# Kernel optimization log

Measured on AMD Instinct MI355X. Metric: run time of the kernel, lower is better.

Reference implementation:

```python
import jax, jax.numpy as jnp
import numpy as np

N_NODES = 50000
HEADS = 3
C = 64  # node_channels
NEG_SLOPE = 0.2


def setup_inputs() -> dict:
    key = jax.random.key(0)
    ks = jax.random.split(key, 8)
    E = 800000
    x = jax.random.normal(ks[0], (N_NODES, C), dtype=jnp.float32)
    edge_index = jax.random.randint(ks[1], (2, E), 0, N_NODES, dtype=jnp.int64)
    edge_attr = jax.random.normal(ks[2], (E, 16), dtype=jnp.float32)
    weight_node = jax.random.normal(ks[3], (C, HEADS * C), dtype=jnp.float32) * 0.1
    weight_edge = jax.random.normal(ks[4], (16, HEADS * C), dtype=jnp.float32) * 0.1
    weight_triplet_att = jax.random.normal(ks[5], (1, HEADS, 3 * C), dtype=jnp.float32) * 0.1
    weight_scale = jax.random.normal(ks[6], (HEADS * C, C), dtype=jnp.float32) * 0.1
    bias = jnp.zeros((C,), dtype=jnp.float32)
    return {"x": x, "edge_index": edge_index, "edge_attr": edge_attr,
            "weight_node": weight_node, "weight_edge": weight_edge,
            "weight_triplet_att": weight_triplet_att,
            "weight_scale": weight_scale, "bias": bias}


def reference(x, edge_index, edge_attr, weight_node, weight_edge,
              weight_triplet_att, weight_scale, bias):
    E = edge_index.shape[1]
    src = edge_index[0]  # j (source)
    dst = edge_index[1]  # i (target, softmax/aggregation index)

    x_proj = x @ weight_node              # [N, H*C]
    e = edge_attr @ weight_edge           # [E, H*C]

    x_j = x_proj[src].reshape(E, HEADS, C)
    x_i = x_proj[dst].reshape(E, HEADS, C)
    e_ij = e.reshape(E, HEADS, C)

    # attention weights split over the triplet concat [x_i | e_ij | x_j]
    w = weight_triplet_att.reshape(HEADS, 3, C)  # [H,3,C]
    alpha = (jnp.einsum('ehc,hc->eh', x_i, w[:, 0])
             + jnp.einsum('ehc,hc->eh', e_ij, w[:, 1])
             + jnp.einsum('ehc,hc->eh', x_j, w[:, 2]))  # [E,H]
    alpha = jnp.where(alpha >= 0, alpha, NEG_SLOPE * alpha)  # leaky_relu

    # scatter-softmax over incoming edges of each target node
    m = jax.ops.segment_max(alpha, dst, num_segments=N_NODES)  # [N,H]
    m = jnp.where(jnp.isfinite(m), m, 0.0)
    exp_a = jnp.exp(alpha - m[dst])
    denom = jax.ops.segment_sum(exp_a, dst, num_segments=N_NODES)  # [N,H]
    alpha = exp_a / (denom[dst] + 1e-16)

    msg = alpha[:, :, None] * e_ij * x_j  # [E,H,C]
    aggr = jax.ops.segment_sum(msg.reshape(E, HEADS * C), dst,
                               num_segments=N_NODES)  # [N,H*C]
    return aggr @ weight_scale + bias
```

## Files before the change

kernel.cpp:

```cpp
#include <hip/hip_runtime.h>
#include <hip/hip_bf16.h>


#define N_NODES 50000
#define CCH 64
#define HEADS 3
#define HC 192
#define NEG_SLOPE 0.2f
#define NWAVES 12288

typedef _Float16 h2 __attribute__((ext_vector_type(2)));
__device__ __forceinline__ h2 uh(unsigned u) {
    union { unsigned u; h2 h; } x; x.u = u; return x.h;
}
__device__ __forceinline__ unsigned hu(float a, float b) {
    union { unsigned u; _Float16 h[2]; } x;
    x.h[0] = (_Float16)a; x.h[1] = (_Float16)b; return x.u;
}

__global__ __launch_bounds__(256) void k_hist(const int* __restrict__ ei,
                                              int* __restrict__ cnt,
                                              const float* __restrict__ We,
                                              const float* __restrict__ Watt,
                                              float* __restrict__ v1, int E) {
    int e = blockIdx.x * 256 + threadIdx.x;
    if (e < E) atomicAdd(&cnt[ei[E + e]], 1);
    if (blockIdx.x == 0 && threadIdx.x < HEADS * 16) {
        int h = threadIdx.x / 16, k = threadIdx.x % 16;
        float s = 0.f;
        #pragma unroll
        for (int c = 0; c < CCH; ++c)
            s = fmaf(We[k * HC + h * CCH + c], Watt[h * HC + CCH + c], s);
        v1[threadIdx.x] = s;
    }
}

__global__ __launch_bounds__(192) void k_xproj(
    const float* __restrict__ x, const float* __restrict__ Wn,
    const float* __restrict__ Watt, uint2* __restrict__ xph2,
    float* __restrict__ a0, float* __restrict__ a2) {
    __shared__ _Float16 pack[16 * CCH * 4];
    int t = threadIdx.x;
    float wreg[CCH];
    #pragma unroll
    for (int k = 0; k < CCH; ++k) wreg[k] = Wn[k * HC + t];
    int base = blockIdx.x * 16;
    int h = t >> 6, c = t & 63;
    float w0 = Watt[h * HC + c];
    float w2 = Watt[h * HC + 2 * CCH + c];
    int jmax = N_NODES - base; jmax = jmax > 16 ? 16 : jmax;
    #pragma unroll 1
    for (int j = 0; j < jmax; ++j) {
        const float* xr = x + (size_t)(base + j) * CCH;
        float val = 0.f;
        #pragma unroll
        for (int k = 0; k < CCH; ++k) val = fmaf(xr[k], wreg[k], val);
        pack[(j * CCH + c) * 4 + h] = (_Float16)val;
        if (h == 0) pack[(j * CCH + c) * 4 + 3] = (_Float16)0.f;
        float p0 = val * w0, p2 = val * w2;
        #pragma unroll
        for (int off = 32; off; off >>= 1) {
            p0 += __shfl_down(p0, off);
            p2 += __shfl_down(p2, off);
        }
        if (c == 0) {
            a0[(base + j) * HEADS + h] = p0;
            a2[(base + j) * HEADS + h] = p2;
        }
    }
    __syncthreads();
    const uint2* p2v = (const uint2*)pack;
    for (int i = t; i < 16 * CCH; i += 192) {
        int n = base + (i >> 6);
        if (n < N_NODES) xph2[(size_t)base * CCH + i] = p2v[i];
    }
}

__global__ __launch_bounds__(1024) void k_bsum(const int* __restrict__ cnt,
                                               int* __restrict__ bsum) {
    __shared__ int ws[16];
    int t = threadIdx.x, lane = t & 63, wid = t >> 6;
    int i = blockIdx.x * 1024 + t;
    int v = (i < N_NODES) ? cnt[i] : 0;
    #pragma unroll
    for (int o = 32; o; o >>= 1) v += __shfl_down(v, o);
    if (lane == 0) ws[wid] = v;
    __syncthreads();
    if (wid == 0) {
        int s = (lane < 16) ? ws[lane] : 0;
        #pragma unroll
        for (int o = 8; o; o >>= 1) s += __shfl_down(s, o);
        if (lane == 0) bsum[blockIdx.x] = s;
    }
}

__global__ __launch_bounds__(1024) void k_fin(const int* __restrict__ cnt,
                                              const int* __restrict__ bsum,
                                              int* __restrict__ off,
                                              int* __restrict__ cursor) {
    __shared__ int ws[16];
    __shared__ int bof_s;
    int t = threadIdx.x, lane = t & 63, wid = t >> 6;
    int i = blockIdx.x * 1024 + t;
    int v = (i < N_NODES) ? cnt[i] : 0;
    int x = v;
    #pragma unroll
    for (int o = 1; o < 64; o <<= 1) {
        int y = __shfl_up(x, o);
        if (lane >= o) x += y;
    }
    if (lane == 63) ws[wid] = x;
    __syncthreads();
    if (wid == 0) {
        int s = (lane < 16) ? ws[lane] : 0;
        #pragma unroll
        for (int o = 1; o < 16; o <<= 1) {
            int y = __shfl_up(s, o);
            if (lane >= o) s += y;
        }
        if (lane < 16) ws[lane] = s;
    } else if (wid == 1) {
        int bv = (lane < 49) ? bsum[lane] : 0;
        int bx = bv;
        #pragma unroll
        for (int o = 1; o < 64; o <<= 1) {
            int y = __shfl_up(bx, o);
            if (lane >= o) bx += y;
        }
        if (lane == (int)blockIdx.x) bof_s = bx - bv;
        if (blockIdx.x == 48 && lane == 48) off[N_NODES] = bx;
    }
    __syncthreads();
    int excl = bof_s + (wid ? ws[wid - 1] : 0) + x - v;
    if (i < N_NODES) { off[i] = excl; cursor[i] = excl; }
}

__global__ __launch_bounds__(256) void k_part(const int* __restrict__ off,
                                              int* __restrict__ wstart, int E) {
    int w = blockIdx.x * 256 + threadIdx.x;
    if (w > NWAVES) return;
    if (w == NWAVES) { wstart[NWAVES] = N_NODES; return; }
    long tgt = (long)E * w / NWAVES;
    int lo = 0, hi = N_NODES;
    while (lo < hi) {
        int mid = (lo + hi) >> 1;
        if (off[mid] < (int)tgt) lo = mid + 1; else hi = mid;
    }
    wstart[w] = lo;
}

__global__ __launch_bounds__(256) void k_place(
    const int* __restrict__ ei, const float* __restrict__ ea,
    const float* __restrict__ a0, const float* __restrict__ a2,
    const float* __restrict__ v1, int* __restrict__ cursor,
    float* __restrict__ recs, int E) {
    int e = blockIdx.x * 256 + threadIdx.x;
    if (e >= E) return;
    int src = ei[e], dst = ei[E + e];
    const float4* q = (const float4*)(ea + (size_t)e * 16);
    float4 q0 = q[0], q1 = q[1], q2 = q[2], q3 = q[3];
    float at[16] = {q0.x, q0.y, q0.z, q0.w, q1.x, q1.y, q1.z, q1.w,
                    q2.x, q2.y, q2.z, q2.w, q3.x, q3.y, q3.z, q3.w};
    float ex[HEADS];
    #pragma unroll
    for (int h = 0; h < HEADS; ++h) {
        float s = a0[dst * HEADS + h] + a2[src * HEADS + h];
        #pragma unroll
        for (int j = 0; j < 16; ++j) s = fmaf(at[j], v1[h * 16 + j], s);
        s = (s >= 0.f) ? s : NEG_SLOPE * s;
        ex[h] = __expf(s);
    }
    int pos = atomicAdd(&cursor[dst], 1);
    float* rp = recs + (size_t)pos * 12;
    uint4 r0 = {hu(at[0], at[1]), hu(at[2], at[3]), hu(at[4], at[5]), hu(at[6], at[7])};
    uint4 r1 = {hu(at[8], at[9]), hu(at[10], at[11]), hu(at[12], at[13]), hu(at[14], at[15])};
    float4 r2 = {ex[0], ex[1], ex[2], __int_as_float(src)};
    *(uint4*)rp = r0;
    *(uint4*)(rp + 4) = r1;
    *(float4*)(rp + 8) = r2;
}

__global__ __launch_bounds__(256, 6) void k_msg(
    const int* __restrict__ off, const int* __restrict__ wstart,
    const float* __restrict__ recs, const uint2* __restrict__ xph2,
    const float* __restrict__ We, _Float16* __restrict__ rowsH) {
    int lane = threadIdx.x & 63;
    int w = blockIdx.x * 4 + (threadIdx.x >> 6);
    #define WP(h, q) hu(We[(2*(q)) * HC + (h) * CCH + lane], \
                        We[(2*(q)+1) * HC + (h) * CCH + lane])
    unsigned w00 = WP(0,0), w01 = WP(0,1), w02 = WP(0,2), w03 = WP(0,3),
             w04 = WP(0,4), w05 = WP(0,5), w06 = WP(0,6), w07 = WP(0,7);
    unsigned w10 = WP(1,0), w11 = WP(1,1), w12 = WP(1,2), w13 = WP(1,3),
             w14 = WP(1,4), w15 = WP(1,5), w16 = WP(1,6), w17 = WP(1,7);
    unsigned w20 = WP(2,0), w21 = WP(2,1), w22 = WP(2,2), w23 = WP(2,3),
             w24 = WP(2,4), w25 = WP(2,5), w26 = WP(2,6), w27 = WP(2,7);
    #undef WP

    int n0 = wstart[w], n1 = wstart[w + 1];
    n0 = __builtin_amdgcn_readfirstlane(n0);
    n1 = __builtin_amdgcn_readfirstlane(n1);
    if (n0 >= n1) return;

    int n = n0;
    int k    = __builtin_amdgcn_readfirstlane(off[n0]);
    int kend = __builtin_amdgcn_readfirstlane(off[n1]);
    int re   = __builtin_amdgcn_readfirstlane(off[n0 + 1]);

    float acc0 = 0.f, acc1 = 0.f, acc2 = 0.f;
    float den0 = 0.f, den1 = 0.f, den2 = 0.f;

    uint4 U0, U1; float4 RX; uint2 xv;
    if (k < kend) {
        const float* rp = recs + (size_t)k * 12;
        U0 = *(const uint4*)rp;
        U1 = *(const uint4*)(rp + 4);
        RX = *(const float4*)(rp + 8);
        int src = __builtin_amdgcn_readfirstlane(__float_as_int(RX.w));
        xv = xph2[(size_t)src * CCH + lane];
    }

    #define FLUSH(nn)                                                      \
        {                                                                  \
            size_t ro = (size_t)(nn) * HC + lane;                          \
            rowsH[ro]           = (_Float16)(acc0 / (den0 + 1e-16f));      \
            rowsH[ro + CCH]     = (_Float16)(acc1 / (den1 + 1e-16f));      \
            rowsH[ro + 2 * CCH] = (_Float16)(acc2 / (den2 + 1e-16f));      \
            acc0 = acc1 = acc2 = den0 = den1 = den2 = 0.f;                 \
        }

    while (k < kend) {
        while (k == re) {
            FLUSH(n);
            ++n;
            re = __builtin_amdgcn_readfirstlane(off[n + 1]);
        }
        int kn = (k + 1 < kend) ? k + 1 : k;
        const float* rpn = recs + (size_t)kn * 12;
        uint4 U0n = *(const uint4*)rpn;
        uint4 U1n = *(const uint4*)(rpn + 4);
        float4 RXn = *(const float4*)(rpn + 8);
        float ev0 = 0.f, ev1 = 0.f, ev2 = 0.f;
        #define D(u, wv, acc) acc = __builtin_amdgcn_fdot2(uh(u), uh(wv), acc, false);
        D(U0.x, w00, ev0) D(U0.x, w10, ev1) D(U0.x, w20, ev2)
        D(U0.y, w01, ev0) D(U0.y, w11, ev1) D(U0.y, w21, ev2)
        D(U0.z, w02, ev0) D(U0.z, w12, ev1) D(U0.z, w22, ev2)
        D(U0.w, w03, ev0) D(U0.w, w13, ev1) D(U0.w, w23, ev2)
        D(U1.x, w04, ev0) D(U1.x, w14, ev1) D(U1.x, w24, ev2)
        D(U1.y, w05, ev0) D(U1.y, w15, ev1) D(U1.y, w25, ev2)
        D(U1.z, w06, ev0) D(U1.z, w16, ev1) D(U1.z, w26, ev2)
        D(U1.w, w07, ev0) D(U1.w, w17, ev1) D(U1.w, w27, ev2)
        #undef D
        h2 xa = uh(xv.x), xb = uh(xv.y);
        den0 += RX.x; den1 += RX.y; den2 += RX.z;
        acc0 = fmaf(RX.x * ev0, (float)xa.x, acc0);
        acc1 = fmaf(RX.y * ev1, (float)xa.y, acc1);
        acc2 = fmaf(RX.z * ev2, (float)xb.x, acc2);
        U0 = U0n; U1 = U1n; RX = RXn;
        int src_n = __builtin_amdgcn_readfirstlane(__float_as_int(RXn.w));
        xv = xph2[(size_t)src_n * CCH + lane];
        ++k;
    }
    FLUSH(n);
    while (++n < n1) FLUSH(n);
    #undef FLUSH
}

__global__ __launch_bounds__(256) void k_out(
    const _Float16* __restrict__ rowsH, const float* __restrict__ Ws,
    const float* __restrict__ bias, float* __restrict__ out) {
    int lane = threadIdx.x & 63;
    int wgid = __builtin_amdgcn_readfirstlane(blockIdx.x * 4 + (threadIdx.x >> 6));
    float b = bias[lane];
    #define WQ(q) hu(Ws[(2*(q)) * CCH + lane], Ws[(2*(q)+1) * CCH + lane])
    unsigned s00=WQ(0),  s01=WQ(1),  s02=WQ(2),  s03=WQ(3),  s04=WQ(4),  s05=WQ(5),  s06=WQ(6),  s07=WQ(7);
    unsigned s08=WQ(8),  s09=WQ(9),  s10=WQ(10), s11=WQ(11), s12=WQ(12), s13=WQ(13), s14=WQ(14), s15=WQ(15);
    unsigned s16=WQ(16), s17=WQ(17), s18=WQ(18), s19=WQ(19), s20=WQ(20), s21=WQ(21), s22=WQ(22), s23=WQ(23);
    unsigned s24=WQ(24), s25=WQ(25), s26=WQ(26), s27=WQ(27), s28=WQ(28), s29=WQ(29), s30=WQ(30), s31=WQ(31);
    unsigned s32=WQ(32), s33=WQ(33), s34=WQ(34), s35=WQ(35), s36=WQ(36), s37=WQ(37), s38=WQ(38), s39=WQ(39);
    unsigned s40=WQ(40), s41=WQ(41), s42=WQ(42), s43=WQ(43), s44=WQ(44), s45=WQ(45), s46=WQ(46), s47=WQ(47);
    unsigned s48=WQ(48), s49=WQ(49), s50=WQ(50), s51=WQ(51), s52=WQ(52), s53=WQ(53), s54=WQ(54), s55=WQ(55);
    unsigned s56=WQ(56), s57=WQ(57), s58=WQ(58), s59=WQ(59), s60=WQ(60), s61=WQ(61), s62=WQ(62), s63=WQ(63);
    unsigned s64=WQ(64), s65=WQ(65), s66=WQ(66), s67=WQ(67), s68=WQ(68), s69=WQ(69), s70=WQ(70), s71=WQ(71);
    unsigned s72=WQ(72), s73=WQ(73), s74=WQ(74), s75=WQ(75), s76=WQ(76), s77=WQ(77), s78=WQ(78), s79=WQ(79);
    unsigned s80=WQ(80), s81=WQ(81), s82=WQ(82), s83=WQ(83), s84=WQ(84), s85=WQ(85), s86=WQ(86), s87=WQ(87);
    unsigned s88=WQ(88), s89=WQ(89), s90=WQ(90), s91=WQ(91), s92=WQ(92), s93=WQ(93), s94=WQ(94), s95=WQ(95);
    #undef WQ
    #pragma unroll 1
    for (int n = wgid; n < N_NODES; n += 1024) {
        const unsigned* rp = (const unsigned*)(rowsH + (size_t)n * HC);
        float a0_ = b, a1_ = 0.f, a2_ = 0.f, a3_ = 0.f;
        #define DQ(q, sreg, acc) acc = __builtin_amdgcn_fdot2(uh(rp[q]), uh(sreg), acc, false);
        DQ(0,s00,a0_)  DQ(1,s01,a1_)  DQ(2,s02,a2_)  DQ(3,s03,a3_)
        DQ(4,s04,a0_)  DQ(5,s05,a1_)  DQ(6,s06,a2_)  DQ(7,s07,a3_)
        DQ(8,s08,a0_)  DQ(9,s09,a1_)  DQ(10,s10,a2_) DQ(11,s11,a3_)
        DQ(12,s12,a0_) DQ(13,s13,a1_) DQ(14,s14,a2_) DQ(15,s15,a3_)
        DQ(16,s16,a0_) DQ(17,s17,a1_) DQ(18,s18,a2_) DQ(19,s19,a3_)
        DQ(20,s20,a0_) DQ(21,s21,a1_) DQ(22,s22,a2_) DQ(23,s23,a3_)
        DQ(24,s24,a0_) DQ(25,s25,a1_) DQ(26,s26,a2_) DQ(27,s27,a3_)
        DQ(28,s28,a0_) DQ(29,s29,a1_) DQ(30,s30,a2_) DQ(31,s31,a3_)
        DQ(32,s32,a0_) DQ(33,s33,a1_) DQ(34,s34,a2_) DQ(35,s35,a3_)
        DQ(36,s36,a0_) DQ(37,s37,a1_) DQ(38,s38,a2_) DQ(39,s39,a3_)
        DQ(40,s40,a0_) DQ(41,s41,a1_) DQ(42,s42,a2_) DQ(43,s43,a3_)
        DQ(44,s44,a0_) DQ(45,s45,a1_) DQ(46,s46,a2_) DQ(47,s47,a3_)
        DQ(48,s48,a0_) DQ(49,s49,a1_) DQ(50,s50,a2_) DQ(51,s51,a3_)
        DQ(52,s52,a0_) DQ(53,s53,a1_) DQ(54,s54,a2_) DQ(55,s55,a3_)
        DQ(56,s56,a0_) DQ(57,s57,a1_) DQ(58,s58,a2_) DQ(59,s59,a3_)
        DQ(60,s60,a0_) DQ(61,s61,a1_) DQ(62,s62,a2_) DQ(63,s63,a3_)
        DQ(64,s64,a0_) DQ(65,s65,a1_) DQ(66,s66,a2_) DQ(67,s67,a3_)
        DQ(68,s68,a0_) DQ(69,s69,a1_) DQ(70,s70,a2_) DQ(71,s71,a3_)
        DQ(72,s72,a0_) DQ(73,s73,a1_) DQ(74,s74,a2_) DQ(75,s75,a3_)
        DQ(76,s76,a0_) DQ(77,s77,a1_) DQ(78,s78,a2_) DQ(79,s79,a3_)
        DQ(80,s80,a0_) DQ(81,s81,a1_) DQ(82,s82,a2_) DQ(83,s83,a3_)
        DQ(84,s84,a0_) DQ(85,s85,a1_) DQ(86,s86,a2_) DQ(87,s87,a3_)
        DQ(88,s88,a0_) DQ(89,s89,a1_) DQ(90,s90,a2_) DQ(91,s91,a3_)
        DQ(92,s92,a0_) DQ(93,s93,a1_) DQ(94,s94,a2_) DQ(95,s95,a3_)
        #undef DQ
        out[(size_t)n * CCH + lane] = (a0_ + a1_) + (a2_ + a3_);
    }
}

extern "C" void kernel_launch(void* const* d_in, const int* in_sizes, int n_in,
                              void* d_out, int out_size, void* d_ws, size_t ws_size,
                              hipStream_t stream) {
    const float* x    = (const float*)d_in[0];
    const int*   ei   = (const int*)d_in[1];
    const float* ea   = (const float*)d_in[2];
    const float* Wn   = (const float*)d_in[3];
    const float* We   = (const float*)d_in[4];
    const float* Watt = (const float*)d_in[5];
    const float* Ws   = (const float*)d_in[6];
    const float* bias = (const float*)d_in[7];
    float* out = (float*)d_out;

    const int E = in_sizes[1] / 2;

    char* w = (char*)d_ws;
    size_t o = 0;
    int*   cnt    = (int*)(w + o);    o += 50048 * 4;
    int*   off    = (int*)(w + o);    o += 50064 * 4;
    int*   cursor = (int*)(w + o);    o += 50048 * 4;
    int*   wst    = (int*)(w + o);    o += (NWAVES + 16) * 4;
    int*   bsum   = (int*)(w + o);    o += 64 * 4;
    float* v1     = (float*)(w + o);  o += 64 * 4;
    float* a0     = (float*)(w + o);  o += 150016 * 4;
    float* a2     = (float*)(w + o);  o += 150016 * 4;
    uint2* xph2   = (uint2*)(w + o);  o += (size_t)N_NODES * CCH * 8;
    _Float16* rowsH = (_Float16*)(w + o); o += (size_t)N_NODES * HC * 2;
    float* recs   = (float*)(w + o);  o += (size_t)E * 48;

    hipMemsetAsync(cnt, 0, 50048 * 4, stream);

    k_hist<<<(E + 255) / 256, 256, 0, stream>>>(ei, cnt, We, Watt, v1, E);
    k_xproj<<<(N_NODES + 15) / 16, 192, 0, stream>>>(x, Wn, Watt, xph2, a0, a2);
    k_bsum<<<49, 1024, 0, stream>>>(cnt, bsum);
    k_fin<<<49, 1024, 0, stream>>>(cnt, bsum, off, cursor);
    k_part<<<(NWAVES + 256) / 256, 256, 0, stream>>>(off, wst, E);
    k_place<<<(E + 255) / 256, 256, 0, stream>>>(ei, ea, a0, a2, v1, cursor, recs, E);
    k_msg<<<NWAVES / 4, 256, 0, stream>>>(off, wst, recs, xph2, We, rowsH);
    k_out<<<256, 256, 0, stream>>>(rowsH, Ws, bias, out);
}
```

Measured before the change: 377.2 us.

## Merge histogram with node projection and fuse scan stages via grid barrier

Folds the degree histogram and v1 precompute into the node projection kernel as extra blocks, and fuses the block-sum, prefix-scan finish and wave partition kernels into one 49-block kernel that uses a software grid barrier. This cuts the launch count from eight to five and removes the gaps between small dependent kernels. The grid barrier assumes all 49 blocks are co-resident, which holds on this GPU, and it adds atomic spin waiting.

```diff
diff --git a/kernel.cpp b/kernel.cpp
--- a/kernel.cpp
+++ b/kernel.cpp
@@ -8,6 +8,8 @@
 #define HC 192
 #define NEG_SLOPE 0.2f
 #define NWAVES 12288
+#define NBX 3125
+#define NSCAN 49
 
 typedef _Float16 h2 __attribute__((ext_vector_type(2)));
 __device__ __forceinline__ h2 uh(unsigned u) {
@@ -18,33 +20,45 @@
     x.h[0] = (_Float16)a; x.h[1] = (_Float16)b; return x.u;
 }
 
-__global__ __launch_bounds__(256) void k_hist(const int* __restrict__ ei,
-                                              int* __restrict__ cnt,
-                                              const float* __restrict__ We,
-                                              const float* __restrict__ Watt,
-                                              float* __restrict__ v1, int E) {
-    int e = blockIdx.x * 256 + threadIdx.x;
-    if (e < E) atomicAdd(&cnt[ei[E + e]], 1);
-    if (blockIdx.x == 0 && threadIdx.x < HEADS * 16) {
-        int h = threadIdx.x / 16, k = threadIdx.x % 16;
-        float s = 0.f;
-        #pragma unroll
-        for (int c = 0; c < CCH; ++c)
-            s = fmaf(We[k * HC + h * CCH + c], Watt[h * HC + CCH + c], s);
-        v1[threadIdx.x] = s;
-    }
-}
-
-__global__ __launch_bounds__(192) void k_xproj(
+__device__ __forceinline__ void gbar(int* bar, int phase, int nb) {
+    __syncthreads();
+    if (threadIdx.x == 0) {
+        __threadfence();
+        __hip_atomic_fetch_add(&bar[phase], 1, __ATOMIC_ACQ_REL,
+                               __HIP_MEMORY_SCOPE_AGENT);
+        while (__hip_atomic_load(&bar[phase], __ATOMIC_ACQUIRE,
+                                 __HIP_MEMORY_SCOPE_AGENT) < nb) {}
+        __threadfence();
+    }
+    __syncthreads();
+}
+
+__global__ __launch_bounds__(192) void k_front(
     const float* __restrict__ x, const float* __restrict__ Wn,
     const float* __restrict__ Watt, uint2* __restrict__ xph2,
-    float* __restrict__ a0, float* __restrict__ a2) {
+    float* __restrict__ a0, float* __restrict__ a2,
+    const int* __restrict__ ei, int* __restrict__ cnt,
+    const float* __restrict__ We, float* __restrict__ v1, int E) {
+    int t = threadIdx.x;
+    int bx = blockIdx.x;
+    if (bx >= NBX) {
+        int e = (bx - NBX) * 192 + t;
+        if (e < E) atomicAdd(&cnt[ei[E + e]], 1);
+        if (bx == NBX && t < HEADS * 16) {
+            int h = t / 16, k = t % 16;
+            float s = 0.f;
+            #pragma unroll
+            for (int c = 0; c < CCH; ++c)
+                s = fmaf(We[k * HC + h * CCH + c], Watt[h * HC + CCH + c], s);
+            v1[t] = s;
+        }
+        return;
+    }
     __shared__ _Float16 pack[16 * CCH * 4];
-    int t = threadIdx.x;
     float wreg[CCH];
     #pragma unroll
     for (int k = 0; k < CCH; ++k) wreg[k] = Wn[k * HC + t];
-    int base = blockIdx.x * 16;
+    int base = bx * 16;
     int h = t >> 6, c = t & 63;
     float w0 = Watt[h * HC + c];
     float w2 = Watt[h * HC + 2 * CCH + c];
@@ -76,33 +90,29 @@
     }
 }
 
-__global__ __launch_bounds__(1024) void k_bsum(const int* __restrict__ cnt,
-                                               int* __restrict__ bsum) {
-    __shared__ int ws[16];
-    int t = threadIdx.x, lane = t & 63, wid = t >> 6;
-    int i = blockIdx.x * 1024 + t;
-    int v = (i < N_NODES) ? cnt[i] : 0;
-    #pragma unroll
-    for (int o = 32; o; o >>= 1) v += __shfl_down(v, o);
-    if (lane == 0) ws[wid] = v;
-    __syncthreads();
-    if (wid == 0) {
-        int s = (lane < 16) ? ws[lane] : 0;
-        #pragma unroll
-        for (int o = 8; o; o >>= 1) s += __shfl_down(s, o);
-        if (lane == 0) bsum[blockIdx.x] = s;
-    }
-}
-
-__global__ __launch_bounds__(1024) void k_fin(const int* __restrict__ cnt,
-                                              const int* __restrict__ bsum,
-                                              int* __restrict__ off,
-                                              int* __restrict__ cursor) {
+__global__ __launch_bounds__(1024) void k_scan49(
+    const int* __restrict__ cnt, int* __restrict__ off, int* __restrict__ cursor,
+    int* __restrict__ wstart, int* __restrict__ bar, int* __restrict__ bsum,
+    int E) {
     __shared__ int ws[16];
     __shared__ int bof_s;
-    int t = threadIdx.x, lane = t & 63, wid = t >> 6;
-    int i = blockIdx.x * 1024 + t;
+    int b = blockIdx.x, t = threadIdx.x, lane = t & 63, wid = t >> 6;
+    int i = b * 1024 + t;
     int v = (i < N_NODES) ? cnt[i] : 0;
+    {
+        int r = v;
+        #pragma unroll
+        for (int o = 32; o; o >>= 1) r += __shfl_down(r, o);
+        if (lane == 0) ws[wid] = r;
+        __syncthreads();
+        if (wid == 0) {
+            int s = (lane < 16) ? ws[lane] : 0;
+            #pragma unroll
+            for (int o = 8; o; o >>= 1) s += __shfl_down(s, o);
+            if (lane == 0) bsum[b] = s;
+        }
+    }
+    gbar(bar, 0, NSCAN);
     int x = v;
     #pragma unroll
     for (int o = 1; o < 64; o <<= 1) {
@@ -120,33 +130,33 @@
         }
         if (lane < 16) ws[lane] = s;
     } else if (wid == 1) {
-        int bv = (lane < 49) ? bsum[lane] : 0;
+        int bv = (lane < NSCAN) ? bsum[lane] : 0;
         int bx = bv;
         #pragma unroll
         for (int o = 1; o < 64; o <<= 1) {
             int y = __shfl_up(bx, o);
             if (lane >= o) bx += y;
         }
-        if (lane == (int)blockIdx.x) bof_s = bx - bv;
-        if (blockIdx.x == 48 && lane == 48) off[N_NODES] = bx;
+        if (lane == b) bof_s = bx - bv;
     }
     __syncthreads();
     int excl = bof_s + (wid ? ws[wid - 1] : 0) + x - v;
     if (i < N_NODES) { off[i] = excl; cursor[i] = excl; }
-}
-
-__global__ __launch_bounds__(256) void k_part(const int* __restrict__ off,
-                                              int* __restrict__ wstart, int E) {
-    int w = blockIdx.x * 256 + threadIdx.x;
-    if (w > NWAVES) return;
-    if (w == NWAVES) { wstart[NWAVES] = N_NODES; return; }
-    long tgt = (long)E * w / NWAVES;
-    int lo = 0, hi = N_NODES;
-    while (lo < hi) {
-        int mid = (lo + hi) >> 1;
-        if (off[mid] < (int)tgt) lo = mid + 1; else hi = mid;
-    }
-    wstart[w] = lo;
+    if (b == 0 && t == 0) off[N_NODES] = E;
+    gbar(bar, 1, NSCAN);
+    int w = i;
+    if (w <= NWAVES) {
+        if (w == NWAVES) { wstart[NWAVES] = N_NODES; }
+        else {
+            long tgt = (long)E * w / NWAVES;
+            int lo = 0, hi = N_NODES;
+            while (lo < hi) {
+                int mid = (lo + hi) >> 1;
+                if (off[mid] < (int)tgt) lo = mid + 1; else hi = mid;
+            }
+            wstart[w] = lo;
+        }
+    }
 }
 
 __global__ __launch_bounds__(256) void k_place(
@@ -337,6 +347,7 @@
     char* w = (char*)d_ws;
     size_t o = 0;
     int*   cnt    = (int*)(w + o);    o += 50048 * 4;
+    int*   bar    = (int*)(w + o);    o += 16 * 4;
     int*   off    = (int*)(w + o);    o += 50064 * 4;
     int*   cursor = (int*)(w + o);    o += 50048 * 4;
     int*   wst    = (int*)(w + o);    o += (NWAVES + 16) * 4;
@@ -348,13 +359,12 @@
     _Float16* rowsH = (_Float16*)(w + o); o += (size_t)N_NODES * HC * 2;
     float* recs   = (float*)(w + o);  o += (size_t)E * 48;
 
-    hipMemsetAsync(cnt, 0, 50048 * 4, stream);
-
-    k_hist<<<(E + 255) / 256, 256, 0, stream>>>(ei, cnt, We, Watt, v1, E);
-    k_xproj<<<(N_NODES + 15) / 16, 192, 0, stream>>>(x, Wn, Watt, xph2, a0, a2);
-    k_bsum<<<49, 1024, 0, stream>>>(cnt, bsum);
-    k_fin<<<49, 1024, 0, stream>>>(cnt, bsum, off, cursor);
-    k_part<<<(NWAVES + 256) / 256, 256, 0, stream>>>(off, wst, E);
+    hipMemsetAsync(cnt, 0, (50048 + 16) * 4, stream);
+
+    const int nbh = (E + 191) / 192;
+    k_front<<<NBX + nbh, 192, 0, stream>>>(x, Wn, Watt, xph2, a0, a2,
+                                           ei, cnt, We, v1, E);
+    k_scan49<<<NSCAN, 1024, 0, stream>>>(cnt, off, cursor, wst, bar, bsum, E);
     k_place<<<(E + 255) / 256, 256, 0, stream>>>(ei, ea, a0, a2, v1, cursor, recs, E);
     k_msg<<<NWAVES / 4, 256, 0, stream>>>(off, wst, recs, xph2, We, rowsH);
     k_out<<<256, 256, 0, stream>>>(rowsH, Ws, bias, out);
```

New measurement: 372.1 us. About the same (-1.4%).
